# Performance work log

Measured on AMD Instinct MI355X. Metric: run time of the kernel, lower is better.

Reference implementation:

```python
import jax, jax.numpy as jnp
import numpy as np

NHEAD = 16
EPS_L1 = 1e-12
LN_EPS = 1e-5


def _layernorm(x, g, b):
    mu = jnp.mean(x, axis=-1, keepdims=True)
    var = jnp.mean(jnp.square(x - mu), axis=-1, keepdims=True)
    return (x - mu) / jnp.sqrt(var + LN_EPS) * g + b


def setup_inputs() -> dict:
    key = jax.random.key(0)
    ks = jax.random.split(key, 16)
    S, B, E, P, F = 2048, 2, 1024, 64, 4096
    sc = lambda n: 1.0 / np.sqrt(n)
    return {
        "src": jax.random.normal(ks[0], (S, B, E), jnp.float32),
        "pos_embed": jax.random.normal(ks[1], (B, P, S), jnp.float32),
        "in_proj_w": jax.random.normal(ks[2], (3 * E, E), jnp.float32) * sc(E),
        "in_proj_b": jnp.zeros((3 * E,), jnp.float32),
        "out_w": jax.random.normal(ks[3], (E, E), jnp.float32) * sc(E),
        "out_b": jnp.zeros((E,), jnp.float32),
        "lin1_w": jax.random.normal(ks[4], (F, E), jnp.float32) * sc(E),
        "lin1_b": jnp.zeros((F,), jnp.float32),
        "lin2_w": jax.random.normal(ks[5], (E, F), jnp.float32) * sc(F),
        "lin2_b": jnp.zeros((E,), jnp.float32),
        "ln1_g": jnp.ones((E,), jnp.float32),
        "ln1_b": jnp.zeros((E,), jnp.float32),
        "ln2_g": jnp.ones((E,), jnp.float32),
        "ln2_b": jnp.zeros((E,), jnp.float32),
        "pos_w": jax.random.normal(ks[6], (P, P), jnp.float32) * sc(P),
        "pos_b": jnp.zeros((P,), jnp.float32),
    }


def reference(src, pos_embed, in_proj_w, in_proj_b, out_w, out_b,
              lin1_w, lin1_b, lin2_w, lin2_b,
              ln1_g, ln1_b, ln2_g, ln2_b, pos_w, pos_b):
    S, B, E = src.shape
    H = NHEAD
    Dh = E // H

    # --- custom positional-similarity kernel (cosine_similarity w/ L1 norm) ---
    pe = jnp.einsum('bps,qp->bqs', pos_embed, pos_w) + pos_b[None, :, None]  # learnable pos
    l1 = jnp.maximum(jnp.sum(jnp.abs(pe), axis=1, keepdims=True), EPS_L1)
    pe = pe / l1                                                # [B,P,S]
    pos_sim = jnp.einsum('bps,bpt->bst', pe, pe)                # [B,S,S]

    # --- manual multi-head self-attention ---
    qkv = src @ in_proj_w.T + in_proj_b                          # [S,B,3E]
    q, k, v = jnp.split(qkv, 3, axis=-1)
    q = q * (Dh ** -0.5)
    to_bhsd = lambda t: jnp.transpose(t.reshape(S, B, H, Dh), (1, 2, 0, 3))
    q, k, v = to_bhsd(q), to_bhsd(k), to_bhsd(v)                 # [B,H,S,Dh]
    scores = jnp.einsum('bhsd,bhtd->bhst', q, k) + pos_sim[:, None]
    attn = jax.nn.softmax(scores, axis=-1)                       # [B,H,S,S]
    ctx = jnp.einsum('bhst,bhtd->bhsd', attn, v)                 # [B,H,S,Dh]
    ctx = jnp.transpose(ctx, (2, 0, 1, 3)).reshape(S, B, E)
    attn_out = ctx @ out_w.T + out_b

    # --- residual + norm + FFN (post-norm, relu) ---
    x = _layernorm(src + attn_out, ln1_g, ln1_b)
    ff = jax.nn.relu(x @ lin1_w.T + lin1_b) @ lin2_w.T + lin2_b
    return _layernorm(x + ff, ln2_g, ln2_b)
```

## Files before the change

kernel.cpp:

```cpp
#include <hip/hip_runtime.h>
#include <hip/hip_bf16.h>
#include <math.h>

#define S_LEN 2048
#define BATCH 2
#define EMB   1024
#define NH    16
#define DH    64
#define E3    3072
#define FF    4096
#define PP    64

typedef __bf16 bf16x8 __attribute__((ext_vector_type(8)));
typedef float  floatx4 __attribute__((ext_vector_type(4)));

__device__ __forceinline__ void load_lds16(const void* g, void* l) {
  __builtin_amdgcn_global_load_lds(
      (const __attribute__((address_space(1))) void*)g,
      (__attribute__((address_space(3))) void*)l, 16, 0, 0);
}

__global__ __launch_bounds__(256) void cvt_kernel(
    const float* __restrict__ in, __hip_bfloat16* __restrict__ out, int n)
{
  int i = (blockIdx.x * 256 + threadIdx.x) * 8;
  if (i >= n) return;
  float4 a = *(const float4*)&in[i];
  float4 b = *(const float4*)&in[i + 4];
  __hip_bfloat16 t[8];
  t[0] = __float2bfloat16(a.x); t[1] = __float2bfloat16(a.y);
  t[2] = __float2bfloat16(a.z); t[3] = __float2bfloat16(a.w);
  t[4] = __float2bfloat16(b.x); t[5] = __float2bfloat16(b.y);
  t[6] = __float2bfloat16(b.z); t[7] = __float2bfloat16(b.w);
  *(float4*)&out[i] = *(float4*)t;
}

__global__ __launch_bounds__(64) void pe_kernel(
    const float* __restrict__ pos_embed, const float* __restrict__ pos_w,
    const float* __restrict__ pos_b, __hip_bfloat16* __restrict__ peT)
{
  __shared__ float pw[PP * PP];
  int tid = threadIdx.x;
  for (int i = 0; i < PP; ++i) pw[i * PP + tid] = pos_w[i * PP + tid];
  __syncthreads();
  int s = blockIdx.x * 64 + tid;
  int b = blockIdx.y;
  float acc[PP];
#pragma unroll
  for (int q = 0; q < PP; ++q) acc[q] = pos_b[q];
  for (int p = 0; p < PP; ++p) {
    float x = pos_embed[(size_t)(b * PP + p) * S_LEN + s];
#pragma unroll
    for (int q = 0; q < PP; ++q) acc[q] += pw[q * PP + p] * x;
  }
  float l1 = 0.f;
#pragma unroll
  for (int q = 0; q < PP; ++q) l1 += fabsf(acc[q]);
  float inv = 1.f / fmaxf(l1, 1e-12f);
  __hip_bfloat16 tmp[PP];
#pragma unroll
  for (int q = 0; q < PP; ++q) tmp[q] = __float2bfloat16(acc[q] * inv);
  float4* dst = (float4*)&peT[((size_t)b * S_LEN + s) * PP];
#pragma unroll
  for (int i = 0; i < 8; ++i) dst[i] = ((float4*)tmp)[i];
}

template <int WR, int WC>
__global__ __launch_bounds__(256) void gemm_bf16(
    const __hip_bfloat16* __restrict__ A, const __hip_bfloat16* __restrict__ W,
    const float* __restrict__ bias, float* __restrict__ Cf,
    __hip_bfloat16* __restrict__ Cb, int M, int N, int K, int relu, int qkscale,
    long strideA, long strideW, long strideC)
{
  constexpr int BM = 2 * WR * 16;
  constexpr int BN = 2 * WC * 16;
  __shared__ __bf16 As[BM * 64];
  __shared__ __bf16 Bs[BN * 64];
  A += (size_t)blockIdx.z * strideA;
  W += (size_t)blockIdx.z * strideW;
  int tid = threadIdx.x;
  int bm = blockIdx.y * BM;
  int bn = blockIdx.x * BN;
  int wave = tid >> 6, lane = tid & 63;
  int wm = (wave & 1) * (WR * 16), wn = (wave >> 1) * (WC * 16);
  int srow = tid >> 3, scb = tid & 7;
  int gcb = scb ^ (srow & 7);
  const __hip_bfloat16* Ap = A + (size_t)(bm + srow) * K + gcb * 8;
  const __hip_bfloat16* Wp = W + (size_t)(bn + srow) * K + gcb * 8;
  __bf16* AsBase = As + tid * 8;
  __bf16* BsBase = Bs + tid * 8;
  int r15 = lane & 15, quad = lane >> 4;

  floatx4 acc[WR * WC];
#pragma unroll
  for (int i = 0; i < WR * WC; ++i) acc[i] = (floatx4){0.f, 0.f, 0.f, 0.f};

  for (int k0 = 0; k0 < K; k0 += 64) {
    __syncthreads();
#pragma unroll
    for (int io = 0; io < BM / 32; ++io)
      load_lds16(Ap + (size_t)(32 * io) * K + k0, AsBase + io * 2048);
#pragma unroll
    for (int io = 0; io < BN / 32; ++io)
      load_lds16(Wp + (size_t)(32 * io) * K + k0, BsBase + io * 2048);
    __syncthreads();
#pragma unroll
    for (int kc = 0; kc < 2; ++kc) {
      bf16x8 af[WR], bfv[WC];
      int kb = kc * 4 + quad;
#pragma unroll
      for (int i = 0; i < WR; ++i) {
        int rowa = wm + i * 16 + r15;
        af[i] = *(const bf16x8*)&As[rowa * 64 + (kb ^ (rowa & 7)) * 8];
      }
#pragma unroll
      for (int j = 0; j < WC; ++j) {
        int rowb = wn + j * 16 + r15;
        bfv[j] = *(const bf16x8*)&Bs[rowb * 64 + (kb ^ (rowb & 7)) * 8];
      }
#pragma unroll
      for (int i = 0; i < WR; ++i)
#pragma unroll
        for (int j = 0; j < WC; ++j)
          acc[i * WC + j] = __builtin_amdgcn_mfma_f32_16x16x32_bf16(
              af[i], bfv[j], acc[i * WC + j], 0, 0, 0);
    }
  }
  int crow0 = bm + wm + quad * 4;
  int ccol0 = bn + wn + r15;
  float* CfB = Cf ? Cf + (size_t)blockIdx.z * strideC : nullptr;
  __hip_bfloat16* CbB = Cb ? Cb + (size_t)blockIdx.z * strideC : nullptr;
#pragma unroll
  for (int j = 0; j < WC; ++j) {
    int col = ccol0 + j * 16;
    float bv = bias ? bias[col] : 0.f;
    float scale = (qkscale && col < EMB) ? 0.125f : 1.f;
#pragma unroll
    for (int i = 0; i < WR; ++i) {
#pragma unroll
      for (int r = 0; r < 4; ++r) {
        int row = crow0 + i * 16 + r;
        float v = (acc[i * WC + j][r] + bv) * scale;
        if (relu) v = fmaxf(v, 0.f);
        if (CfB) CfB[(size_t)row * N + col] = v;
        if (CbB) CbB[(size_t)row * N + col] = __float2bfloat16(v);
      }
    }
  }
}

__global__ __launch_bounds__(256) void transpose_v(
    const __hip_bfloat16* __restrict__ qkv, __hip_bfloat16* __restrict__ vT)
{
  __shared__ __hip_bfloat16 tile[64][72];
  int c0 = blockIdx.x * 64, t0 = blockIdx.y * 64, b = blockIdx.z;
  int tid = threadIdx.x;
#pragma unroll
  for (int i = 0; i < 2; ++i) {
    int k = tid * 2 + i;
    int row = k >> 3, col = (k & 7) * 8;
    float4 v = *(const float4*)&qkv[((size_t)(t0 + row) * BATCH + b) * E3 + 2 * EMB + c0 + col];
    __hip_bfloat16 tmp[8];
    *(float4*)tmp = v;
#pragma unroll
    for (int j = 0; j < 8; ++j) tile[row][col + j] = tmp[j];
  }
  __syncthreads();
#pragma unroll
  for (int i = 0; i < 2; ++i) {
    int k = tid * 2 + i;
    int crow = k >> 3, tcol = (k & 7) * 8;
    __hip_bfloat16 tmp[8];
#pragma unroll
    for (int j = 0; j < 8; ++j) tmp[j] = tile[tcol + j][crow];
    *(float4*)&vT[((size_t)(b * EMB + c0 + crow)) * S_LEN + t0 + tcol] = *(float4*)tmp;
  }
}

__global__ __launch_bounds__(256) void attn_mfma(
    const __hip_bfloat16* __restrict__ qkv,
    const __hip_bfloat16* __restrict__ vT,
    const float* __restrict__ pos_sim,
    __hip_bfloat16* __restrict__ ctx)
{
  __shared__ __bf16 Ks[2][4096];
  __shared__ __bf16 Vs[2][4096];
  __shared__ __bf16 Ps[8192];
  int tid = threadIdx.x;
  int q0 = blockIdx.x * 128, h = blockIdx.y, b = blockIdx.z;
  int w = tid >> 6, lane = tid & 63, quad = lane >> 4, r15 = lane & 15;
  int srow = tid >> 3, scb = tid & 7;
  int x7 = r15 & 7;

  const __hip_bfloat16* kbase = qkv + EMB + (size_t)h * DH;
  const __hip_bfloat16* vbase = vT + ((size_t)b * EMB + h * DH) * S_LEN;

  bf16x8 qa[2][2];
#pragma unroll
  for (int qb = 0; qb < 2; ++qb)
#pragma unroll
    for (int kc = 0; kc < 2; ++kc)
      qa[qb][kc] = *(const bf16x8*)&qkv[
          ((size_t)(q0 + w * 32 + qb * 16 + r15) * BATCH + b) * E3 +
          h * DH + kc * 32 + quad * 8];

#pragma unroll
  for (int i = 0; i < 2; ++i) {
    int row = i * 32 + srow;
    int gcb = scb ^ (row & 7);
    load_lds16(kbase + ((size_t)row * BATCH + b) * E3 + gcb * 8,
               Ks[0] + i * 2048 + tid * 8);
    load_lds16(vbase + (size_t)row * S_LEN + gcb * 8,
               Vs[0] + i * 2048 + tid * 8);
  }
  __syncthreads();

  floatx4 of[2][4];
#pragma unroll
  for (int qb = 0; qb < 2; ++qb)
#pragma unroll
    for (int j = 0; j < 4; ++j) of[qb][j] = (floatx4){0.f, 0.f, 0.f, 0.f};
  float lp[2] = {0.f, 0.f};

  const float* psb[2];
#pragma unroll
  for (int qb = 0; qb < 2; ++qb)
    psb[qb] = pos_sim + ((size_t)(b * S_LEN + q0 + w * 32 + qb * 16 + r15)) * S_LEN
              + quad * 4;
  __bf16* pw0 = Ps + (w * 2 + 0) * 1024;
  __bf16* pw1 = Ps + (w * 2 + 1) * 1024;

  for (int kt = 0; kt < 32; ++kt) {
    int cur = kt & 1;
    int t0 = kt * 64;
    floatx4 sf[2][4];
#pragma unroll
    for (int qb = 0; qb < 2; ++qb)
#pragma unroll
      for (int j = 0; j < 4; ++j)
        sf[qb][j] = *(const floatx4*)(psb[qb] + t0 + j * 16);
    if (kt < 31) {
      int tn = t0 + 64;
      int nb = cur ^ 1;
#pragma unroll
      for (int i = 0; i < 2; ++i) {
        int row = i * 32 + srow;
        int gcb = scb ^ (row & 7);
        load_lds16(kbase + ((size_t)(tn + row) * BATCH + b) * E3 + gcb * 8,
                   Ks[nb] + i * 2048 + tid * 8);
        load_lds16(vbase + (size_t)row * S_LEN + tn + gcb * 8,
                   Vs[nb] + i * 2048 + tid * 8);
      }
    }

#pragma unroll
    for (int j = 0; j < 4; ++j) {
      int rowk = j * 16 + r15;
      bf16x8 kf0 = *(const bf16x8*)&Ks[cur][rowk * 64 + (quad ^ (rowk & 7)) * 8];
      bf16x8 kf1 = *(const bf16x8*)&Ks[cur][rowk * 64 + ((4 + quad) ^ (rowk & 7)) * 8];
#pragma unroll
      for (int qb = 0; qb < 2; ++qb) {
        sf[qb][j] = __builtin_amdgcn_mfma_f32_16x16x32_bf16(kf0, qa[qb][0], sf[qb][j], 0, 0, 0);
        sf[qb][j] = __builtin_amdgcn_mfma_f32_16x16x32_bf16(kf1, qa[qb][1], sf[qb][j], 0, 0, 0);
      }
    }

#pragma unroll
    for (int qb = 0; qb < 2; ++qb) {
      __bf16* pwq = qb ? pw1 : pw0;
#pragma unroll
      for (int j = 0; j < 4; ++j) {
        float e0 = __expf(fminf(sf[qb][j][0], 60.f));
        float e1 = __expf(fminf(sf[qb][j][1], 60.f));
        float e2 = __expf(fminf(sf[qb][j][2], 60.f));
        float e3 = __expf(fminf(sf[qb][j][3], 60.f));
        lp[qb] += (e0 + e1) + (e2 + e3);
        __hip_bfloat16 t4[4];
        t4[0] = __float2bfloat16(e0); t4[1] = __float2bfloat16(e1);
        t4[2] = __float2bfloat16(e2); t4[3] = __float2bfloat16(e3);
        int addr = r15 * 64 + (((j * 2 + (quad >> 1)) ^ x7) * 8) + (quad & 1) * 4;
        *(float2*)&pwq[addr] = *(float2*)t4;
      }
    }
    __asm__ volatile("s_waitcnt lgkmcnt(0)" ::: "memory");

    bf16x8 pb00 = *(const bf16x8*)&pw0[r15 * 64 + ((quad ^ x7) * 8)];
    bf16x8 pb01 = *(const bf16x8*)&pw0[r15 * 64 + (((4 + quad) ^ x7) * 8)];
    bf16x8 pb10 = *(const bf16x8*)&pw1[r15 * 64 + ((quad ^ x7) * 8)];
    bf16x8 pb11 = *(const bf16x8*)&pw1[r15 * 64 + (((4 + quad) ^ x7) * 8)];
#pragma unroll
    for (int jd = 0; jd < 4; ++jd) {
      int rowd = jd * 16 + r15;
      bf16x8 vb0 = *(const bf16x8*)&Vs[cur][rowd * 64 + (quad ^ (rowd & 7)) * 8];
      bf16x8 vb1 = *(const bf16x8*)&Vs[cur][rowd * 64 + ((4 + quad) ^ (rowd & 7)) * 8];
      of[0][jd] = __builtin_amdgcn_mfma_f32_16x16x32_bf16(vb0, pb00, of[0][jd], 0, 0, 0);
      of[0][jd] = __builtin_amdgcn_mfma_f32_16x16x32_bf16(vb1, pb01, of[0][jd], 0, 0, 0);
      of[1][jd] = __builtin_amdgcn_mfma_f32_16x16x32_bf16(vb0, pb10, of[1][jd], 0, 0, 0);
      of[1][jd] = __builtin_amdgcn_mfma_f32_16x16x32_bf16(vb1, pb11, of[1][jd], 0, 0, 0);
    }
    __syncthreads();
  }

#pragma unroll
  for (int qb = 0; qb < 2; ++qb) {
    float l = lp[qb];
    l += __shfl_xor(l, 16, 64);
    l += __shfl_xor(l, 32, 64);
    float inv = 1.f / l;
    size_t rbase = ((size_t)(q0 + w * 32 + qb * 16 + r15) * BATCH + b) * EMB + h * DH;
#pragma unroll
    for (int jd = 0; jd < 4; ++jd) {
      __hip_bfloat16 o4[4];
      o4[0] = __float2bfloat16(of[qb][jd][0] * inv);
      o4[1] = __float2bfloat16(of[qb][jd][1] * inv);
      o4[2] = __float2bfloat16(of[qb][jd][2] * inv);
      o4[3] = __float2bfloat16(of[qb][jd][3] * inv);
      *(float2*)&ctx[rbase + jd * 16 + quad * 4] = *(float2*)o4;
    }
  }
}

__global__ __launch_bounds__(256) void ln_kernel(
    const float* __restrict__ x1, const float* __restrict__ x2,
    const float* __restrict__ g, const float* __restrict__ bb,
    float* __restrict__ out, __hip_bfloat16* __restrict__ out_bf)
{
  int row = blockIdx.x;
  int tid = threadIdx.x;
  const float* p1 = x1 + (size_t)row * EMB;
  const float* p2 = x2 + (size_t)row * EMB;
  float4 v1 = *(const float4*)&p1[tid * 4];
  float4 v2 = *(const float4*)&p2[tid * 4];
  float x[4] = {v1.x + v2.x, v1.y + v2.y, v1.z + v2.z, v1.w + v2.w};
  float s = x[0] + x[1] + x[2] + x[3];
  float s2 = x[0] * x[0] + x[1] * x[1] + x[2] * x[2] + x[3] * x[3];
#pragma unroll
  for (int off = 32; off >= 1; off >>= 1) {
    s  += __shfl_xor(s, off, 64);
    s2 += __shfl_xor(s2, off, 64);
  }
  __shared__ float ws1[4], ws2[4];
  int wid = tid >> 6, lane = tid & 63;
  if (lane == 0) { ws1[wid] = s; ws2[wid] = s2; }
  __syncthreads();
  s  = ws1[0] + ws1[1] + ws1[2] + ws1[3];
  s2 = ws2[0] + ws2[1] + ws2[2] + ws2[3];
  float mean = s * (1.f / EMB);
  float var  = s2 * (1.f / EMB) - mean * mean;
  float inv  = rsqrtf(var + 1e-5f);
  float4 gv = *(const float4*)&g[tid * 4];
  float4 bv = *(const float4*)&bb[tid * 4];
  float4 o;
  o.x = (x[0] - mean) * inv * gv.x + bv.x;
  o.y = (x[1] - mean) * inv * gv.y + bv.y;
  o.z = (x[2] - mean) * inv * gv.z + bv.z;
  o.w = (x[3] - mean) * inv * gv.w + bv.w;
  *(float4*)&out[(size_t)row * EMB + tid * 4] = o;
  if (out_bf) {
    __hip_bfloat16 t[4];
    t[0] = __float2bfloat16(o.x); t[1] = __float2bfloat16(o.y);
    t[2] = __float2bfloat16(o.z); t[3] = __float2bfloat16(o.w);
    *(float2*)&out_bf[(size_t)row * EMB + tid * 4] = *(float2*)t;
  }
}

extern "C" void kernel_launch(void* const* d_in, const int* in_sizes, int n_in,
                              void* d_out, int out_size, void* d_ws, size_t ws_size,
                              hipStream_t stream)
{
  const float* src       = (const float*)d_in[0];
  const float* pos_embed = (const float*)d_in[1];
  const float* in_proj_w = (const float*)d_in[2];
  const float* in_proj_b = (const float*)d_in[3];
  const float* out_w     = (const float*)d_in[4];
  const float* out_b     = (const float*)d_in[5];
  const float* lin1_w    = (const float*)d_in[6];
  const float* lin1_b    = (const float*)d_in[7];
  const float* lin2_w    = (const float*)d_in[8];
  const float* lin2_b    = (const float*)d_in[9];
  const float* ln1_g     = (const float*)d_in[10];
  const float* ln1_b     = (const float*)d_in[11];
  const float* ln2_g     = (const float*)d_in[12];
  const float* ln2_b     = (const float*)d_in[13];
  const float* pos_w     = (const float*)d_in[14];
  const float* pos_b     = (const float*)d_in[15];
  float* out = (float*)d_out;
  float* ws  = (float*)d_ws;

  __hip_bfloat16* peT    = (__hip_bfloat16*)ws;
  float* pos_sim         = ws + 131072;
  __hip_bfloat16* qkv_bf = (__hip_bfloat16*)(ws + 8519680);
  __hip_bfloat16* vT_bf  = (__hip_bfloat16*)(ws + 14811136);
  __hip_bfloat16* src_bf = (__hip_bfloat16*)(ws + 16908288);
  __hip_bfloat16* inw_bf  = (__hip_bfloat16*)(ws + 19005440);
  __hip_bfloat16* outw_bf = (__hip_bfloat16*)(ws + 20578304);
  __hip_bfloat16* ctx_bf = (__hip_bfloat16*)(ws + 21102592);
  __hip_bfloat16* l1w_bf = (__hip_bfloat16*)(ws + 23199744);
  __hip_bfloat16* l2w_bf = (__hip_bfloat16*)(ws + 25296896);
  float* proj            = ws + 27394048;
  __hip_bfloat16* x_bf   = (__hip_bfloat16*)ws;
  float* xbuf            = ws + 2097152;
  __hip_bfloat16* h1_bf  = (__hip_bfloat16*)(ws + 6291456);

  const int M = S_LEN * BATCH;

  cvt_kernel<<<4194304 / 2048, 256, 0, stream>>>(src, src_bf, 4194304);
  cvt_kernel<<<3145728 / 2048, 256, 0, stream>>>(in_proj_w, inw_bf, 3145728);
  cvt_kernel<<<1048576 / 2048, 256, 0, stream>>>(out_w, outw_bf, 1048576);
  cvt_kernel<<<4194304 / 2048, 256, 0, stream>>>(lin1_w, l1w_bf, 4194304);
  cvt_kernel<<<4194304 / 2048, 256, 0, stream>>>(lin2_w, l2w_bf, 4194304);
  pe_kernel<<<dim3(S_LEN / 64, BATCH), 64, 0, stream>>>(pos_embed, pos_w, pos_b, peT);
  gemm_bf16<4, 4><<<dim3(2048 / 128, 2048 / 128, BATCH), 256, 0, stream>>>(
      peT, peT, nullptr, pos_sim, nullptr, 2048, 2048, 64, 0, 0,
      (long)2048 * 64, (long)2048 * 64, (long)2048 * 2048);
  gemm_bf16<4, 4><<<dim3(E3 / 128, M / 128, 1), 256, 0, stream>>>(
      src_bf, inw_bf, in_proj_b, nullptr, qkv_bf, M, E3, EMB, 0, 1, 0, 0, 0);
  transpose_v<<<dim3(EMB / 64, S_LEN / 64, BATCH), 256, 0, stream>>>(qkv_bf, vT_bf);
  attn_mfma<<<dim3(S_LEN / 128, NH, BATCH), 256, 0, stream>>>(
      qkv_bf, vT_bf, pos_sim, ctx_bf);
  gemm_bf16<2, 4><<<dim3(EMB / 128, M / 64, 1), 256, 0, stream>>>(
      ctx_bf, outw_bf, out_b, proj, nullptr, M, EMB, EMB, 0, 0, 0, 0, 0);
  ln_kernel<<<dim3(M), 256, 0, stream>>>(src, proj, ln1_g, ln1_b, xbuf, x_bf);
  gemm_bf16<4, 4><<<dim3(FF / 128, M / 128, 1), 256, 0, stream>>>(
      x_bf, l1w_bf, lin1_b, nullptr, h1_bf, M, FF, EMB, 1, 0, 0, 0, 0);
  gemm_bf16<2, 4><<<dim3(EMB / 128, M / 64, 1), 256, 0, stream>>>(
      h1_bf, l2w_bf, lin2_b, proj, nullptr, M, EMB, FF, 0, 0, 0, 0, 0);
  ln_kernel<<<dim3(M), 256, 0, stream>>>(xbuf, proj, ln2_g, ln2_b, out, nullptr);
}
```

Measured before the change: 460.1 us.

## Fuse positional similarity into attention by concatenating pe to Q and K

Drops the separate pos_sim GEMM and its 2x2048x2048 fp32 matrix, which the attention kernel had to read from global memory for every score tile. Each query row now carries its L1-normalised positional vector as 64 extra contraction dimensions. Matching pe tiles are streamed into LDS next to K, so the bias comes from two extra MFMAs per tile. This removes about 32 MB of pos_sim writes and reads, at the cost of doubled QK MFMA work, more LDS and register pressure, and a bf16 rather than fp32 positional bias. The workspace pointer edits for x_bf and xbuf are overwritten back to their old values.

```diff
diff --git a/kernel.cpp b/kernel.cpp
--- a/kernel.cpp
+++ b/kernel.cpp
@@ -180,10 +180,11 @@
 __global__ __launch_bounds__(256) void attn_mfma(
     const __hip_bfloat16* __restrict__ qkv,
     const __hip_bfloat16* __restrict__ vT,
-    const float* __restrict__ pos_sim,
+    const __hip_bfloat16* __restrict__ peT,
     __hip_bfloat16* __restrict__ ctx)
 {
   __shared__ __bf16 Ks[2][4096];
+  __shared__ __bf16 Kp[2][4096];
   __shared__ __bf16 Vs[2][4096];
   __shared__ __bf16 Ps[8192];
   int tid = threadIdx.x;
@@ -194,15 +195,21 @@
 
   const __hip_bfloat16* kbase = qkv + EMB + (size_t)h * DH;
   const __hip_bfloat16* vbase = vT + ((size_t)b * EMB + h * DH) * S_LEN;
-
-  bf16x8 qa[2][2];
-#pragma unroll
-  for (int qb = 0; qb < 2; ++qb)
+  const __hip_bfloat16* pbase = peT + (size_t)b * S_LEN * PP;
+
+  bf16x8 qa[2][4];
+#pragma unroll
+  for (int qb = 0; qb < 2; ++qb) {
+    int qrow = q0 + w * 32 + qb * 16 + r15;
 #pragma unroll
     for (int kc = 0; kc < 2; ++kc)
       qa[qb][kc] = *(const bf16x8*)&qkv[
-          ((size_t)(q0 + w * 32 + qb * 16 + r15) * BATCH + b) * E3 +
-          h * DH + kc * 32 + quad * 8];
+          ((size_t)qrow * BATCH + b) * E3 + h * DH + kc * 32 + quad * 8];
+#pragma unroll
+    for (int kc = 0; kc < 2; ++kc)
+      qa[qb][2 + kc] = *(const bf16x8*)&pbase[
+          (size_t)qrow * PP + kc * 32 + quad * 8];
+  }
 
 #pragma unroll
   for (int i = 0; i < 2; ++i) {
@@ -210,6 +217,8 @@
     int gcb = scb ^ (row & 7);
     load_lds16(kbase + ((size_t)row * BATCH + b) * E3 + gcb * 8,
                Ks[0] + i * 2048 + tid * 8);
+    load_lds16(pbase + (size_t)row * PP + gcb * 8,
+               Kp[0] + i * 2048 + tid * 8);
     load_lds16(vbase + (size_t)row * S_LEN + gcb * 8,
                Vs[0] + i * 2048 + tid * 8);
   }
@@ -222,23 +231,12 @@
     for (int j = 0; j < 4; ++j) of[qb][j] = (floatx4){0.f, 0.f, 0.f, 0.f};
   float lp[2] = {0.f, 0.f};
 
-  const float* psb[2];
-#pragma unroll
-  for (int qb = 0; qb < 2; ++qb)
-    psb[qb] = pos_sim + ((size_t)(b * S_LEN + q0 + w * 32 + qb * 16 + r15)) * S_LEN
-              + quad * 4;
   __bf16* pw0 = Ps + (w * 2 + 0) * 1024;
   __bf16* pw1 = Ps + (w * 2 + 1) * 1024;
 
   for (int kt = 0; kt < 32; ++kt) {
     int cur = kt & 1;
     int t0 = kt * 64;
-    floatx4 sf[2][4];
-#pragma unroll
-    for (int qb = 0; qb < 2; ++qb)
-#pragma unroll
-      for (int j = 0; j < 4; ++j)
-        sf[qb][j] = *(const floatx4*)(psb[qb] + t0 + j * 16);
     if (kt < 31) {
       int tn = t0 + 64;
       int nb = cur ^ 1;
@@ -248,20 +246,32 @@
         int gcb = scb ^ (row & 7);
         load_lds16(kbase + ((size_t)(tn + row) * BATCH + b) * E3 + gcb * 8,
                    Ks[nb] + i * 2048 + tid * 8);
+        load_lds16(pbase + (size_t)(tn + row) * PP + gcb * 8,
+                   Kp[nb] + i * 2048 + tid * 8);
         load_lds16(vbase + (size_t)row * S_LEN + tn + gcb * 8,
                    Vs[nb] + i * 2048 + tid * 8);
       }
     }
 
+    floatx4 sf[2][4];
+#pragma unroll
+    for (int qb = 0; qb < 2; ++qb)
+#pragma unroll
+      for (int j = 0; j < 4; ++j) sf[qb][j] = (floatx4){0.f, 0.f, 0.f, 0.f};
 #pragma unroll
     for (int j = 0; j < 4; ++j) {
       int rowk = j * 16 + r15;
-      bf16x8 kf0 = *(const bf16x8*)&Ks[cur][rowk * 64 + (quad ^ (rowk & 7)) * 8];
-      bf16x8 kf1 = *(const bf16x8*)&Ks[cur][rowk * 64 + ((4 + quad) ^ (rowk & 7)) * 8];
+      int rx = rowk & 7;
+      bf16x8 kf0 = *(const bf16x8*)&Ks[cur][rowk * 64 + ((quad ^ rx)) * 8];
+      bf16x8 kf1 = *(const bf16x8*)&Ks[cur][rowk * 64 + (((4 + quad) ^ rx)) * 8];
+      bf16x8 kp0 = *(const bf16x8*)&Kp[cur][rowk * 64 + ((quad ^ rx)) * 8];
+      bf16x8 kp1 = *(const bf16x8*)&Kp[cur][rowk * 64 + (((4 + quad) ^ rx)) * 8];
 #pragma unroll
       for (int qb = 0; qb < 2; ++qb) {
         sf[qb][j] = __builtin_amdgcn_mfma_f32_16x16x32_bf16(kf0, qa[qb][0], sf[qb][j], 0, 0, 0);
         sf[qb][j] = __builtin_amdgcn_mfma_f32_16x16x32_bf16(kf1, qa[qb][1], sf[qb][j], 0, 0, 0);
+        sf[qb][j] = __builtin_amdgcn_mfma_f32_16x16x32_bf16(kp0, qa[qb][2], sf[qb][j], 0, 0, 0);
+        sf[qb][j] = __builtin_amdgcn_mfma_f32_16x16x32_bf16(kp1, qa[qb][3], sf[qb][j], 0, 0, 0);
       }
     }
 
@@ -388,7 +398,6 @@
   float* ws  = (float*)d_ws;
 
   __hip_bfloat16* peT    = (__hip_bfloat16*)ws;
-  float* pos_sim         = ws + 131072;
   __hip_bfloat16* qkv_bf = (__hip_bfloat16*)(ws + 8519680);
   __hip_bfloat16* vT_bf  = (__hip_bfloat16*)(ws + 14811136);
   __hip_bfloat16* src_bf = (__hip_bfloat16*)(ws + 16908288);
@@ -398,8 +407,10 @@
   __hip_bfloat16* l1w_bf = (__hip_bfloat16*)(ws + 23199744);
   __hip_bfloat16* l2w_bf = (__hip_bfloat16*)(ws + 25296896);
   float* proj            = ws + 27394048;
-  __hip_bfloat16* x_bf   = (__hip_bfloat16*)ws;
-  float* xbuf            = ws + 2097152;
+  __hip_bfloat16* x_bf   = (__hip_bfloat16*)ws + 2097152;
+  float* xbuf            = ws + 2097152 + 2097152 / 1;
+  x_bf = (__hip_bfloat16*)ws;
+  xbuf = ws + 2097152;
   __hip_bfloat16* h1_bf  = (__hip_bfloat16*)(ws + 6291456);
 
   const int M = S_LEN * BATCH;
@@ -410,14 +421,11 @@
   cvt_kernel<<<4194304 / 2048, 256, 0, stream>>>(lin1_w, l1w_bf, 4194304);
   cvt_kernel<<<4194304 / 2048, 256, 0, stream>>>(lin2_w, l2w_bf, 4194304);
   pe_kernel<<<dim3(S_LEN / 64, BATCH), 64, 0, stream>>>(pos_embed, pos_w, pos_b, peT);
-  gemm_bf16<4, 4><<<dim3(2048 / 128, 2048 / 128, BATCH), 256, 0, stream>>>(
-      peT, peT, nullptr, pos_sim, nullptr, 2048, 2048, 64, 0, 0,
-      (long)2048 * 64, (long)2048 * 64, (long)2048 * 2048);
   gemm_bf16<4, 4><<<dim3(E3 / 128, M / 128, 1), 256, 0, stream>>>(
       src_bf, inw_bf, in_proj_b, nullptr, qkv_bf, M, E3, EMB, 0, 1, 0, 0, 0);
   transpose_v<<<dim3(EMB / 64, S_LEN / 64, BATCH), 256, 0, stream>>>(qkv_bf, vT_bf);
   attn_mfma<<<dim3(S_LEN / 128, NH, BATCH), 256, 0, stream>>>(
-      qkv_bf, vT_bf, pos_sim, ctx_bf);
+      qkv_bf, vT_bf, peT, ctx_bf);
   gemm_bf16<2, 4><<<dim3(EMB / 128, M / 64, 1), 256, 0, stream>>>(
       ctx_bf, outw_bf, out_b, proj, nullptr, M, EMB, EMB, 0, 0, 0, 0, 0);
   ln_kernel<<<dim3(M), 256, 0, stream>>>(src, proj, ln1_g, ln1_b, xbuf, x_bf);
```

After: 437.8 us. 4.8% less time.
